# Kernel optimization log

Hardware: AMD Instinct MI355X
Metric: run time of the kernel (lower is better)

The kernel has to match this reference:

```python
import jax, jax.numpy as jnp
import numpy as np

N = 50000        # nodes
E = 800000       # random edges (plus N self-loops added in setup)
DIN = 128        # input_dim
H = 128          # hidden_dim
L = 3            # num_layers
EPS = 1e-5       # BatchNorm1d eps


def _bn(x, gamma, beta):
    # BatchNorm1d in training mode: batch stats over node axis, biased variance
    m = x.mean(axis=0)
    v = jnp.mean((x - m) ** 2, axis=0)
    return (x - m) * jax.lax.rsqrt(v + EPS) * gamma + beta


def setup_inputs() -> dict:
    key = jax.random.key(0)
    ks = jax.random.split(key, 11)
    feats = jax.random.normal(ks[0], (N, DIN), dtype=jnp.float32)
    # edge list with self-loops so every node has degree >= 1 (average pooling divides by degree)
    loops = jnp.arange(N, dtype=jnp.int64)
    src = jnp.concatenate([jax.random.randint(ks[1], (E,), 0, N, dtype=jnp.int64), loops])
    dst = jnp.concatenate([jax.random.randint(ks[2], (E,), 0, N, dtype=jnp.int64), loops])
    s = 0.05
    # per-layer MLP params (num_mlp_layers=2: Linear -> BN -> ReLU -> Linear), layer 0 has DIN==H
    W1 = jax.random.normal(ks[3], (L, DIN, H), dtype=jnp.float32) * s
    b1 = jnp.zeros((L, H), jnp.float32)
    g1 = jnp.ones((L, H), jnp.float32)
    be1 = jnp.zeros((L, H), jnp.float32)
    W2 = jax.random.normal(ks[4], (L, H, H), dtype=jnp.float32) * s
    b2 = jnp.zeros((L, H), jnp.float32)
    # outer BatchNorm1d per GNN layer
    og = jnp.ones((L, H), jnp.float32)
    ob = jnp.zeros((L, H), jnp.float32)
    return {"feats": feats, "W1": W1, "b1": b1, "g1": g1, "be1": be1,
            "W2": W2, "b2": b2, "og": og, "ob": ob, "src": src, "dst": dst}


def reference(feats, W1, b1, g1, be1, W2, b2, og, ob, src, dst):
    n = feats.shape[0]
    # degree = spmm(Adj, ones) -- constant across layers
    deg = jax.ops.segment_sum(jnp.ones(src.shape, jnp.float32), dst, num_segments=n)[:, None]
    h = feats
    for l in range(L):
        # pooled = spmm(Adj, h) via edge gather + segment reduce, then 'average' normalize
        pooled = jax.ops.segment_sum(h[src], dst, num_segments=n) / deg
        # GIN-style 2-layer MLP: Linear -> BN -> ReLU -> Linear
        z = jax.nn.relu(_bn(pooled @ W1[l] + b1[l], g1[l], be1[l]))
        z = z @ W2[l] + b2[l]
        # outer BatchNorm + ReLU
        h = jax.nn.relu(_bn(z, og[l], ob[l]))
    return h
```

## Files before the change

### kernel.cpp

```cpp
#include <hip/hip_runtime.h>
#include <hip/hip_bf16.h>
#include <stdint.h>

typedef _Float16 h16;
typedef h16 h16x2 __attribute__((ext_vector_type(2)));
typedef h16 h16x8 __attribute__((ext_vector_type(8)));
typedef float f32x4 __attribute__((ext_vector_type(4)));

#define HF 128
#define EPS 1e-5f
#define BSH 9
#define BROWS 512
#define BCAP 16384
#define ECHUNK 8192
#define SBANKS 8

union pk32 { uint32_t u; h16x2 h; };

static __device__ __forceinline__ uint32_t pack_h16(float a, float b) {
    pk32 c;
    c.h[0] = (h16)a; c.h[1] = (h16)b;
    return c.u;
}

static __device__ __forceinline__ float sum8(const float* __restrict__ st, int idx) {
    float s = 0.f;
#pragma unroll
    for (int b = 0; b < SBANKS; b++) s += st[b * 256 + idx];
    return s;
}


__global__ __launch_bounds__(256) void k_bscatter(const int* __restrict__ src,
                                                  const int* __restrict__ dst,
                                                  int* __restrict__ gcursor,
                                                  int2* __restrict__ staging, int ne, int nb) {
    __shared__ int h[128], gb[128];
    const int tid = threadIdx.x;
    if (tid < nb) h[tid] = 0;
    __syncthreads();
    const int beg = blockIdx.x * ECHUNK;
    const int end = min(beg + ECHUNK, ne);
    for (int i = beg + tid; i < end; i += 256)
        atomicAdd(&h[dst[i] >> BSH], 1);
    __syncthreads();
    if (tid < nb) {
        int c = h[tid];
        gb[tid] = c ? atomicAdd(&gcursor[tid], c) : 0;
        h[tid] = 0;
    }
    __syncthreads();
    for (int i = beg + tid; i < end; i += 256) {
        int d = dst[i];
        int b = d >> BSH;
        int r = atomicAdd(&h[b], 1);
        staging[(size_t)b * BCAP + gb[b] + r] = make_int2(src[i], d);
    }
}

__global__ __launch_bounds__(256) void k_bbuild(const int2* __restrict__ staging,
                                                const int* __restrict__ gcursor,
                                                int* __restrict__ rowbeg,
                                                int* __restrict__ rowend,
                                                float* __restrict__ deginv,
                                                int* __restrict__ csrsrc, int n) {
    __shared__ int hist[BROWS];
    __shared__ int scan[BROWS];
    const int b = blockIdx.x;
    const int tid = threadIdx.x;
    const int rb = b << BSH;
    const int nrows = min(BROWS, n - rb);
    const int base = b * BCAP;
    const int cnt = gcursor[b];
    hist[tid] = 0; hist[tid + 256] = 0;
    __syncthreads();
    for (int i = tid; i < cnt; i += 256)
        atomicAdd(&hist[staging[base + i].y - rb], 1);
    __syncthreads();
    const int i0 = tid, i1 = tid + 256;
    scan[i0] = hist[i0]; scan[i1] = hist[i1];
    __syncthreads();
    for (int off = 1; off < BROWS; off <<= 1) {
        int v0 = (i0 >= off) ? scan[i0 - off] : 0;
        int v1 = (i1 >= off) ? scan[i1 - off] : 0;
        __syncthreads();
        scan[i0] += v0; scan[i1] += v1;
        __syncthreads();
    }
    for (int r = tid; r < BROWS; r += 256) {
        int c = hist[r];
        int excl = scan[r] - c;
        if (r < nrows) {
            rowbeg[rb + r] = base + excl;
            rowend[rb + r] = base + excl + c;
            deginv[rb + r] = c ? 1.0f / (float)c : 0.f;
        }
        scan[r] = excl;
    }
    __syncthreads();
    for (int i = tid; i < cnt; i += 256) {
        int2 e = staging[base + i];
        int pos = atomicAdd(&scan[e.y - rb], 1);
        csrsrc[base + pos] = e.x;
    }
}

__global__ __launch_bounds__(256) void k_prep(const float* __restrict__ W1,
                                              const float* __restrict__ W2,
                                              h16* __restrict__ wp,
                                              const float* __restrict__ feats,
                                              uint32_t* __restrict__ hbuf, long tot2) {
    const int bid = (int)blockIdx.x;
    if (bid < 384) {
        const int mat = bid >> 6;
        const int idx = ((bid & 63) << 8) + (int)threadIdx.x;
        const int l = mat >> 1;
        const float* Wsrc = (mat & 1) ? (W2 + l * 16384) : (W1 + l * 16384);
        const int nn = idx >> 7, k = idx & 127;
        float w = Wsrc[k * 128 + nn];
        int pos = nn * 128 + ((((k >> 3) ^ (nn & 7))) << 3) + (k & 7);
        wp[mat * 16384 + pos] = (h16)w;
    } else {
        long i = (long)(bid - 384) * 256 + threadIdx.x;
        if (i < tot2) {
            float2 v = ((const float2*)feats)[i];
            hbuf[i] = pack_h16(v.x, v.y);
        }
    }
}

template <int AFF>
__global__ __launch_bounds__(256) void k_spmm(const uint32_t* __restrict__ hp,
                                              const int* __restrict__ rowbeg,
                                              const int* __restrict__ rowend,
                                              const float* __restrict__ deginv,
                                              const float* __restrict__ st,
                                              const float* __restrict__ g,
                                              const float* __restrict__ be,
                                              float inv_n,
                                              const int* __restrict__ csrsrc,
                                              uint32_t* __restrict__ pooled, int n, int np) {
    const int wid  = (int)((blockIdx.x * 256u + threadIdx.x) >> 6);
    const int lane = threadIdx.x & 63;
    if (wid >= np) return;
    const int gg = lane >> 4;
    const int fl = lane & 15;
    uint4* outrow = (uint4*)(pooled + (size_t)wid * 64);
    if (wid >= n) {
        if (gg == 0) outrow[fl] = make_uint4(0u, 0u, 0u, 0u);
        return;
    }

    uint32_t sv[4], cv[4];
    if (AFF) {
        const int c0 = lane * 2, c1 = c0 + 1;
        float m0 = sum8(st, c0) * inv_n, v0 = sum8(st, 128 + c0) * inv_n - m0 * m0;
        float sx = g[c0] * rsqrtf(v0 + EPS), cx = be[c0] - m0 * sx;
        float m1 = sum8(st, c1) * inv_n, v1 = sum8(st, 128 + c1) * inv_n - m1 * m1;
        float sy = g[c1] * rsqrtf(v1 + EPS), cy = be[c1] - m1 * sy;
        uint32_t su = pack_h16(sx, sy);
        uint32_t cu = pack_h16(cx, cy);
#pragma unroll
        for (int w = 0; w < 4; w++) {
            sv[w] = (uint32_t)__shfl((int)su, fl * 4 + w);
            cv[w] = (uint32_t)__shfl((int)cu, fl * 4 + w);
        }
    }

    const h16 z0 = (h16)0.f;
    h16x2 acc[4];
#pragma unroll
    for (int w = 0; w < 4; w++) acc[w] = (h16x2)z0;

    const int beg = rowbeg[wid], end = rowend[wid];
    for (int base = beg; base < end; base += 64) {
        const int rem = end - base;
        const int cnt = rem < 64 ? rem : 64;
        const int off = lane < cnt ? lane : cnt - 1;
        const int idx = csrsrc[base + off];
        for (int j = 0; j < cnt; j += 32) {
            uint4 p[8];
#pragma unroll
            for (int u = 0; u < 8; u++) {
                const int eb = j + u * 4;
                if (eb < cnt) {
                    int ge = eb + gg;
                    int gec = ge < cnt ? ge : cnt - 1;
                    int s = __shfl(idx, gec);
                    p[u] = *(const uint4*)(hp + (size_t)s * 64 + (fl << 2));
                }
            }
#pragma unroll
            for (int u = 0; u < 8; u++) {
                const int eb = j + u * 4;
                if (eb < cnt) {
                    const uint32_t* pw = (const uint32_t*)&p[u];
                    h16x2 v[4];
#pragma unroll
                    for (int w = 0; w < 4; w++) {
                        pk32 t; t.u = pw[w];
                        h16x2 x = t.h;
                        if (AFF) {
                            pk32 s2; s2.u = sv[w];
                            pk32 c2; c2.u = cv[w];
                            x = x * s2.h + c2.h;
                            x[0] = x[0] > z0 ? x[0] : z0;
                            x[1] = x[1] > z0 ? x[1] : z0;
                        }
                        v[w] = x;
                    }
                    if (eb + gg < cnt) {
#pragma unroll
                        for (int w = 0; w < 4; w++) acc[w] = acc[w] + v[w];
                    }
                }
            }
        }
    }

#pragma unroll
    for (int w = 0; w < 4; w++) {
        pk32 t; t.h = acc[w];
        pk32 r1; r1.u = (uint32_t)__shfl_xor((int)t.u, 16);
        t.h = t.h + r1.h;
        pk32 r2; r2.u = (uint32_t)__shfl_xor((int)t.u, 32);
        t.h = t.h + r2.h;
        acc[w] = t.h;
    }

    const float di = deginv[wid];
    uint4 o;
    o.x = pack_h16((float)acc[0][0] * di, (float)acc[0][1] * di);
    o.y = pack_h16((float)acc[1][0] * di, (float)acc[1][1] * di);
    o.z = pack_h16((float)acc[2][0] * di, (float)acc[2][1] * di);
    o.w = pack_h16((float)acc[3][0] * di, (float)acc[3][1] * di);
    if (gg == 0) outrow[fl] = o;
}

template <int MODE>
__global__ __launch_bounds__(256) void k_gemm(const uint32_t* __restrict__ Ap,
                                              const h16* __restrict__ Wp,
                                              const float* __restrict__ bias,
                                              const float* __restrict__ st,
                                              const float* __restrict__ g,
                                              const float* __restrict__ be,
                                              float inv_n,
                                              h16* __restrict__ Y,
                                              float* __restrict__ outstats, int n) {
    __shared__ __align__(16) h16 WT[128 * 128];
    __shared__ float sred[4][128];
    __shared__ float sred2[4][128];
    __shared__ float aff[256];
    const int tid = threadIdx.x;
    const int wave = tid >> 6, lane = tid & 63;

    {
        const char* gsrc = (const char*)Wp + wave * 1024 + lane * 16;
        char* ldst = (char*)&WT[0] + wave * 1024;
#pragma unroll
        for (int i = 0; i < 8; i++) {
            __builtin_amdgcn_global_load_lds(
                (const __attribute__((address_space(1))) uint32_t*)(gsrc + i * 4096),
                (__attribute__((address_space(3))) uint32_t*)(ldst + i * 4096),
                16, 0, 0);
        }
    }
    if (MODE == 1 && tid < 128) {
        float m = sum8(st, tid) * inv_n;
        float v = sum8(st, 128 + tid) * inv_n - m * m;
        float a = g[tid] * rsqrtf(v + EPS);
        aff[tid] = a;
        aff[128 + tid] = be[tid] - m * a;
    }

    const int lrow = lane & 15, quad = lane >> 4;
    const int bx = (int)blockIdx.x * 128;
    int mb[2];
    mb[0] = bx + wave * 16;
    mb[1] = bx + 64 + wave * 16;

    h16x8 ah[2][4];
    uint4 araw[2][4];
#pragma unroll
    for (int rt = 0; rt < 2; rt++) {
        const uint32_t* arow = Ap + (size_t)(mb[rt] + lrow) * 64 + quad * 4;
#pragma unroll
        for (int kt = 0; kt < 4; kt++)
            araw[rt][kt] = *(const uint4*)(arow + kt * 16);
    }

    __syncthreads();

#pragma unroll
    for (int rt = 0; rt < 2; rt++) {
#pragma unroll
        for (int kt = 0; kt < 4; kt++) {
            if (MODE == 0) {
                ah[rt][kt] = *(const h16x8*)&araw[rt][kt];
            } else {
                const uint32_t* pw = (const uint32_t*)&araw[rt][kt];
                h16x8 t;
#pragma unroll
                for (int j2 = 0; j2 < 4; j2++) {
                    pk32 w; w.u = pw[j2];
                    int k = kt * 32 + quad * 8 + j2 * 2;
                    float x0 = fmaxf(fmaf((float)w.h[0], aff[k],     aff[128 + k]),     0.f);
                    float x1 = fmaxf(fmaf((float)w.h[1], aff[k + 1], aff[129 + k]), 0.f);
                    t[2 * j2]     = (h16)x0;
                    t[2 * j2 + 1] = (h16)x1;
                }
                ah[rt][kt] = t;
            }
        }
    }

    f32x4 acc[2][8];
#pragma unroll
    for (int rt = 0; rt < 2; rt++)
#pragma unroll
        for (int nt = 0; nt < 8; nt++) acc[rt][nt] = (f32x4){0.f, 0.f, 0.f, 0.f};

    const int sw = lrow & 7;
#pragma unroll
    for (int nt = 0; nt < 8; nt++) {
        const h16* wbase = &WT[(nt * 16 + lrow) * 128];
#pragma unroll
        for (int kt = 0; kt < 4; kt++) {
            h16x8 bh = *(const h16x8*)(wbase + (((4 * kt + quad) ^ sw) << 3));
#pragma unroll
            for (int rt = 0; rt < 2; rt++)
                acc[rt][nt] = __builtin_amdgcn_mfma_f32_16x16x32_f16(ah[rt][kt], bh, acc[rt][nt], 0, 0, 0);
        }
    }

#pragma unroll
    for (int nt = 0; nt < 8; nt++) {
        int col = nt * 16 + lrow;
        float bv = bias[col];
        float csum = 0.f, csq = 0.f;
#pragma unroll
        for (int rt = 0; rt < 2; rt++) {
#pragma unroll
            for (int r = 0; r < 4; r++) {
                int row = mb[rt] + quad * 4 + r;
                float yv = acc[rt][nt][r] + bv;
                Y[(size_t)row * 128 + col] = (h16)yv;
                if (row < n) { csum += yv; csq += yv * yv; }
            }
        }
        csum += __shfl_xor(csum, 16, 64); csum += __shfl_xor(csum, 32, 64);
        csq  += __shfl_xor(csq,  16, 64); csq  += __shfl_xor(csq,  32, 64);
        if (quad == 0) { sred[wave][col] = csum; sred2[wave][col] = csq; }
    }
    __syncthreads();
    if (tid < 128) {
        float s = sred[0][tid] + sred[1][tid] + sred[2][tid] + sred[3][tid];
        float q = sred2[0][tid] + sred2[1][tid] + sred2[2][tid] + sred2[3][tid];
        const int bank = (int)(blockIdx.x & (SBANKS - 1));
        atomicAdd(&outstats[bank * 256 + tid], s);
        atomicAdd(&outstats[bank * 256 + 128 + tid], q);
    }
}

__global__ __launch_bounds__(256) void k_bnrelu(const uint32_t* __restrict__ Z,
                                                const float* __restrict__ st,
                                                const float* __restrict__ g,
                                                const float* __restrict__ be,
                                                float inv_n,
                                                float* __restrict__ out, long tot2) {
    long i = (long)blockIdx.x * 256 + threadIdx.x;
    if (i >= tot2) return;
    int c = (int)((i * 2) & 127);
    float m0 = sum8(st, c) * inv_n,     v0 = sum8(st, 128 + c) * inv_n - m0 * m0;
    float a0 = g[c] * rsqrtf(v0 + EPS),     c0 = be[c] - m0 * a0;
    float m1 = sum8(st, c + 1) * inv_n, v1 = sum8(st, 129 + c) * inv_n - m1 * m1;
    float a1 = g[c + 1] * rsqrtf(v1 + EPS), c1 = be[c + 1] - m1 * a1;
    pk32 w; w.u = Z[i];
    float2 o;
    o.x = fmaxf(fmaf((float)w.h[0], a0, c0), 0.f);
    o.y = fmaxf(fmaf((float)w.h[1], a1, c1), 0.f);
    ((float2*)out)[i] = o;
}

extern "C" void kernel_launch(void* const* d_in, const int* in_sizes, int n_in,
                              void* d_out, int out_size, void* d_ws, size_t ws_size,
                              hipStream_t stream) {
    const float* feats = (const float*)d_in[0];
    const float* W1    = (const float*)d_in[1];
    const float* b1    = (const float*)d_in[2];
    const float* g1    = (const float*)d_in[3];
    const float* be1   = (const float*)d_in[4];
    const float* W2    = (const float*)d_in[5];
    const float* b2    = (const float*)d_in[6];
    const float* og    = (const float*)d_in[7];
    const float* ob    = (const float*)d_in[8];
    const int*   src   = (const int*)d_in[9];
    const int*   dst   = (const int*)d_in[10];

    const int n  = in_sizes[0] / HF;
    const int ne = in_sizes[9];
    const int np = (n + 127) & ~127;
    const int nb = (n + BROWS - 1) >> BSH;

    char* p = (char*)d_ws;
    auto alloc = [&](size_t bytes) -> char* {
        char* r = p;
        p += (bytes + 511) & ~(size_t)511;
        return r;
    };
    uint32_t* hbuf    = (uint32_t*)alloc((size_t)np * 64 * 4);
    uint32_t* pooled  = (uint32_t*)alloc((size_t)np * 64 * 4);
    uint32_t* ybuf    = (uint32_t*)alloc((size_t)np * 64 * 4);
    uint32_t* zb      = (uint32_t*)alloc((size_t)np * 64 * 4);
    h16*      wprep   = (h16*)     alloc(6 * 16384 * 2);
    float*    deginv  = (float*)   alloc((size_t)n * 4);
    int*      rowbeg  = (int*)     alloc((size_t)n * 4);
    int*      rowend  = (int*)     alloc((size_t)n * 4);
    int*      csrsrc  = (int*)     alloc((size_t)nb * BCAP * 4);
    int2*     staging = (int2*)    alloc((size_t)nb * BCAP * 8);
    char*     zone    = alloc(512 + 6 * SBANKS * 256 * 4);
    int*      gcursor = (int*)zone;
    float*    stats6  = (float*)(zone + 512);

    hipMemsetAsync(zone, 0, 512 + 6 * SBANKS * 256 * 4, stream);

    const long tot2  = (long)n * (HF / 2);
    const int bnb    = (int)((tot2 + 255) / 256);
    const int spmmb  = np / 4;
    const int gemmb  = np / 128;
    const float inv_n = 1.0f / (float)n;
    const int ebk = (ne + ECHUNK - 1) / ECHUNK;
    const int SL = SBANKS * 256;

    k_prep    <<<384 + bnb, 256, 0, stream>>>(W1, W2, wprep, feats, hbuf, tot2);
    k_bscatter<<<ebk, 256, 0, stream>>>(src, dst, gcursor, staging, ne, nb);
    k_bbuild  <<<nb, 256, 0, stream>>>(staging, gcursor, rowbeg, rowend, deginv, csrsrc, n);

    for (int l = 0; l < 3; l++) {
        float* sY = stats6 + (2 * l) * SL;
        float* sZ = stats6 + (2 * l + 1) * SL;
        if (l == 0)
            k_spmm<0><<<spmmb, 256, 0, stream>>>(hbuf, rowbeg, rowend, deginv,
                                                 nullptr, nullptr, nullptr, inv_n,
                                                 csrsrc, pooled, n, np);
        else
            k_spmm<1><<<spmmb, 256, 0, stream>>>(zb, rowbeg, rowend, deginv,
                                                 stats6 + (2 * (l - 1) + 1) * SL,
                                                 og + (l - 1) * HF, ob + (l - 1) * HF, inv_n,
                                                 csrsrc, pooled, n, np);
        k_gemm<0><<<gemmb, 256, 0, stream>>>(pooled,
                                             wprep + (size_t)(2 * l) * 16384,
                                             b1 + l * HF,
                                             nullptr, nullptr, nullptr, inv_n,
                                             (h16*)ybuf, sY, n);
        k_gemm<1><<<gemmb, 256, 0, stream>>>(ybuf,
                                             wprep + (size_t)(2 * l + 1) * 16384,
                                             b2 + l * HF,
                                             sY, g1 + l * HF, be1 + l * HF, inv_n,
                                             (h16*)zb, sZ, n);
    }
    k_bnrelu<<<bnb, 256, 0, stream>>>(zb, stats6 + 5 * SL, og + 2 * HF, ob + 2 * HF,
                                      inv_n, (float*)d_out, tot2);
}
```

Before: 375.0 us.

## Merge prep and edge-scatter kernels, split GEMM columns across 8 waves, vectorize BN

Folds the weight/feature conversion kernel and the edge bucket-scatter kernel into one launch, so one kernel launch goes away and the two independent jobs can run side by side. The GEMM kernels now run 512 threads per block. Each pair of waves shares a row group and splits the 128 output columns in half, which halves the accumulator registers per wave and adds parallelism per block. The cost is that both waves in a pair load the same A rows. The final BN+ReLU kernel now handles four features per thread with wider loads and stores.

```diff
diff --git a/kernel.cpp b/kernel.cpp
--- a/kernel.cpp
+++ b/kernel.cpp
@@ -30,31 +30,55 @@
     return s;
 }
 
-
-__global__ __launch_bounds__(256) void k_bscatter(const int* __restrict__ src,
+__global__ __launch_bounds__(256) void k_prepscat(const float* __restrict__ W1,
+                                                  const float* __restrict__ W2,
+                                                  h16* __restrict__ wp,
+                                                  const float* __restrict__ feats,
+                                                  uint32_t* __restrict__ hbuf, long tot2,
+                                                  const int* __restrict__ src,
                                                   const int* __restrict__ dst,
                                                   int* __restrict__ gcursor,
-                                                  int2* __restrict__ staging, int ne, int nb) {
+                                                  int2* __restrict__ staging, int ne, int nb,
+                                                  int ebk) {
     __shared__ int h[128], gb[128];
+    const int bid = (int)blockIdx.x;
     const int tid = threadIdx.x;
-    if (tid < nb) h[tid] = 0;
-    __syncthreads();
-    const int beg = blockIdx.x * ECHUNK;
-    const int end = min(beg + ECHUNK, ne);
-    for (int i = beg + tid; i < end; i += 256)
-        atomicAdd(&h[dst[i] >> BSH], 1);
-    __syncthreads();
-    if (tid < nb) {
-        int c = h[tid];
-        gb[tid] = c ? atomicAdd(&gcursor[tid], c) : 0;
-        h[tid] = 0;
-    }
-    __syncthreads();
-    for (int i = beg + tid; i < end; i += 256) {
-        int d = dst[i];
-        int b = d >> BSH;
-        int r = atomicAdd(&h[b], 1);
-        staging[(size_t)b * BCAP + gb[b] + r] = make_int2(src[i], d);
+    if (bid < ebk) {
+        if (tid < nb) h[tid] = 0;
+        __syncthreads();
+        const int beg = bid * ECHUNK;
+        const int end = min(beg + ECHUNK, ne);
+        for (int i = beg + tid; i < end; i += 256)
+            atomicAdd(&h[dst[i] >> BSH], 1);
+        __syncthreads();
+        if (tid < nb) {
+            int c = h[tid];
+            gb[tid] = c ? atomicAdd(&gcursor[tid], c) : 0;
+            h[tid] = 0;
+        }
+        __syncthreads();
+        for (int i = beg + tid; i < end; i += 256) {
+            int d = dst[i];
+            int b = d >> BSH;
+            int r = atomicAdd(&h[b], 1);
+            staging[(size_t)b * BCAP + gb[b] + r] = make_int2(src[i], d);
+        }
+    } else if (bid < ebk + 384) {
+        const int wb = bid - ebk;
+        const int mat = wb >> 6;
+        const int idx = ((wb & 63) << 8) + tid;
+        const int l = mat >> 1;
+        const float* Wsrc = (mat & 1) ? (W2 + l * 16384) : (W1 + l * 16384);
+        const int nn = idx >> 7, k = idx & 127;
+        float w = Wsrc[k * 128 + nn];
+        int pos = nn * 128 + ((((k >> 3) ^ (nn & 7))) << 3) + (k & 7);
+        wp[mat * 16384 + pos] = (h16)w;
+    } else {
+        long i = (long)(bid - ebk - 384) * 256 + tid;
+        if (i < tot2) {
+            float2 v = ((const float2*)feats)[i];
+            hbuf[i] = pack_h16(v.x, v.y);
+        }
     }
 }
 
@@ -102,30 +126,6 @@
         int2 e = staging[base + i];
         int pos = atomicAdd(&scan[e.y - rb], 1);
         csrsrc[base + pos] = e.x;
-    }
-}
-
-__global__ __launch_bounds__(256) void k_prep(const float* __restrict__ W1,
-                                              const float* __restrict__ W2,
-                                              h16* __restrict__ wp,
-                                              const float* __restrict__ feats,
-                                              uint32_t* __restrict__ hbuf, long tot2) {
-    const int bid = (int)blockIdx.x;
-    if (bid < 384) {
-        const int mat = bid >> 6;
-        const int idx = ((bid & 63) << 8) + (int)threadIdx.x;
-        const int l = mat >> 1;
-        const float* Wsrc = (mat & 1) ? (W2 + l * 16384) : (W1 + l * 16384);
-        const int nn = idx >> 7, k = idx & 127;
-        float w = Wsrc[k * 128 + nn];
-        int pos = nn * 128 + ((((k >> 3) ^ (nn & 7))) << 3) + (k & 7);
-        wp[mat * 16384 + pos] = (h16)w;
-    } else {
-        long i = (long)(bid - 384) * 256 + threadIdx.x;
-        if (i < tot2) {
-            float2 v = ((const float2*)feats)[i];
-            hbuf[i] = pack_h16(v.x, v.y);
-        }
     }
 }
 
@@ -238,7 +238,7 @@
 }
 
 template <int MODE>
-__global__ __launch_bounds__(256) void k_gemm(const uint32_t* __restrict__ Ap,
+__global__ __launch_bounds__(512) void k_gemm(const uint32_t* __restrict__ Ap,
                                               const h16* __restrict__ Wp,
                                               const float* __restrict__ bias,
                                               const float* __restrict__ st,
@@ -258,10 +258,10 @@
         const char* gsrc = (const char*)Wp + wave * 1024 + lane * 16;
         char* ldst = (char*)&WT[0] + wave * 1024;
 #pragma unroll
-        for (int i = 0; i < 8; i++) {
+        for (int i = 0; i < 4; i++) {
             __builtin_amdgcn_global_load_lds(
-                (const __attribute__((address_space(1))) uint32_t*)(gsrc + i * 4096),
-                (__attribute__((address_space(3))) uint32_t*)(ldst + i * 4096),
+                (const __attribute__((address_space(1))) uint32_t*)(gsrc + i * 8192),
+                (__attribute__((address_space(3))) uint32_t*)(ldst + i * 8192),
                 16, 0, 0);
         }
     }
@@ -274,10 +274,11 @@
     }
 
     const int lrow = lane & 15, quad = lane >> 4;
+    const int rg = wave >> 1, nh = wave & 1;
     const int bx = (int)blockIdx.x * 128;
     int mb[2];
-    mb[0] = bx + wave * 16;
-    mb[1] = bx + 64 + wave * 16;
+    mb[0] = bx + rg * 16;
+    mb[1] = bx + 64 + rg * 16;
 
     h16x8 ah[2][4];
     uint4 araw[2][4];
@@ -314,16 +315,17 @@
         }
     }
 
-    f32x4 acc[2][8];
+    f32x4 acc[2][4];
 #pragma unroll
     for (int rt = 0; rt < 2; rt++)
 #pragma unroll
-        for (int nt = 0; nt < 8; nt++) acc[rt][nt] = (f32x4){0.f, 0.f, 0.f, 0.f};
+        for (int nt = 0; nt < 4; nt++) acc[rt][nt] = (f32x4){0.f, 0.f, 0.f, 0.f};
 
     const int sw = lrow & 7;
 #pragma unroll
-    for (int nt = 0; nt < 8; nt++) {
-        const h16* wbase = &WT[(nt * 16 + lrow) * 128];
+    for (int nt = 0; nt < 4; nt++) {
+        const int ntg = nh * 4 + nt;
+        const h16* wbase = &WT[(ntg * 16 + lrow) * 128];
 #pragma unroll
         for (int kt = 0; kt < 4; kt++) {
             h16x8 bh = *(const h16x8*)(wbase + (((4 * kt + quad) ^ sw) << 3));
@@ -334,8 +336,8 @@
     }
 
 #pragma unroll
-    for (int nt = 0; nt < 8; nt++) {
-        int col = nt * 16 + lrow;
+    for (int nt = 0; nt < 4; nt++) {
+        int col = (nh * 4 + nt) * 16 + lrow;
         float bv = bias[col];
         float csum = 0.f, csq = 0.f;
 #pragma unroll
@@ -350,7 +352,7 @@
         }
         csum += __shfl_xor(csum, 16, 64); csum += __shfl_xor(csum, 32, 64);
         csq  += __shfl_xor(csq,  16, 64); csq  += __shfl_xor(csq,  32, 64);
-        if (quad == 0) { sred[wave][col] = csum; sred2[wave][col] = csq; }
+        if (quad == 0) { sred[rg][col] = csum; sred2[rg][col] = csq; }
     }
     __syncthreads();
     if (tid < 128) {
@@ -367,19 +369,27 @@
                                                 const float* __restrict__ g,
                                                 const float* __restrict__ be,
                                                 float inv_n,
-                                                float* __restrict__ out, long tot2) {
+                                                float* __restrict__ out, long tot4) {
     long i = (long)blockIdx.x * 256 + threadIdx.x;
-    if (i >= tot2) return;
-    int c = (int)((i * 2) & 127);
-    float m0 = sum8(st, c) * inv_n,     v0 = sum8(st, 128 + c) * inv_n - m0 * m0;
-    float a0 = g[c] * rsqrtf(v0 + EPS),     c0 = be[c] - m0 * a0;
-    float m1 = sum8(st, c + 1) * inv_n, v1 = sum8(st, 129 + c) * inv_n - m1 * m1;
-    float a1 = g[c + 1] * rsqrtf(v1 + EPS), c1 = be[c + 1] - m1 * a1;
-    pk32 w; w.u = Z[i];
-    float2 o;
-    o.x = fmaxf(fmaf((float)w.h[0], a0, c0), 0.f);
-    o.y = fmaxf(fmaf((float)w.h[1], a1, c1), 0.f);
-    ((float2*)out)[i] = o;
+    if (i >= tot4) return;
+    int c = (int)((i * 4) & 127);
+    float a[4], cc[4];
+#pragma unroll
+    for (int j = 0; j < 4; j++) {
+        float m = sum8(st, c + j) * inv_n;
+        float v = sum8(st, 128 + c + j) * inv_n - m * m;
+        a[j] = g[c + j] * rsqrtf(v + EPS);
+        cc[j] = be[c + j] - m * a[j];
+    }
+    uint2 w2 = ((const uint2*)Z)[i];
+    pk32 w0; w0.u = w2.x;
+    pk32 w1; w1.u = w2.y;
+    float4 o;
+    o.x = fmaxf(fmaf((float)w0.h[0], a[0], cc[0]), 0.f);
+    o.y = fmaxf(fmaf((float)w0.h[1], a[1], cc[1]), 0.f);
+    o.z = fmaxf(fmaf((float)w1.h[0], a[2], cc[2]), 0.f);
+    o.w = fmaxf(fmaf((float)w1.h[1], a[3], cc[3]), 0.f);
+    ((float4*)out)[i] = o;
 }
 
 extern "C" void kernel_launch(void* const* d_in, const int* in_sizes, int n_in,
@@ -425,15 +435,17 @@
     hipMemsetAsync(zone, 0, 512 + 6 * SBANKS * 256 * 4, stream);
 
     const long tot2  = (long)n * (HF / 2);
+    const long tot4  = tot2 / 2;
     const int bnb    = (int)((tot2 + 255) / 256);
+    const int bnb4   = (int)((tot4 + 255) / 256);
     const int spmmb  = np / 4;
     const int gemmb  = np / 128;
     const float inv_n = 1.0f / (float)n;
     const int ebk = (ne + ECHUNK - 1) / ECHUNK;
     const int SL = SBANKS * 256;
 
-    k_prep    <<<384 + bnb, 256, 0, stream>>>(W1, W2, wprep, feats, hbuf, tot2);
-    k_bscatter<<<ebk, 256, 0, stream>>>(src, dst, gcursor, staging, ne, nb);
+    k_prepscat<<<ebk + 384 + bnb, 256, 0, stream>>>(W1, W2, wprep, feats, hbuf, tot2,
+                                                    src, dst, gcursor, staging, ne, nb, ebk);
     k_bbuild  <<<nb, 256, 0, stream>>>(staging, gcursor, rowbeg, rowend, deginv, csrsrc, n);
 
     for (int l = 0; l < 3; l++) {
@@ -448,17 +460,17 @@
                                                  stats6 + (2 * (l - 1) + 1) * SL,
                                                  og + (l - 1) * HF, ob + (l - 1) * HF, inv_n,
                                                  csrsrc, pooled, n, np);
-        k_gemm<0><<<gemmb, 256, 0, stream>>>(pooled,
+        k_gemm<0><<<gemmb, 512, 0, stream>>>(pooled,
                                              wprep + (size_t)(2 * l) * 16384,
                                              b1 + l * HF,
                                              nullptr, nullptr, nullptr, inv_n,
                                              (h16*)ybuf, sY, n);
-        k_gemm<1><<<gemmb, 256, 0, stream>>>(ybuf,
+        k_gemm<1><<<gemmb, 512, 0, stream>>>(ybuf,
                                              wprep + (size_t)(2 * l + 1) * 16384,
                                              b2 + l * HF,
                                              sY, g1 + l * HF, be1 + l * HF, inv_n,
                                              (h16*)zb, sZ, n);
     }
-    k_bnrelu<<<bnb, 256, 0, stream>>>(zb, stats6 + 5 * SL, og + 2 * HF, ob + 2 * HF,
-                                      inv_n, (float*)d_out, tot2);
-}
+    k_bnrelu<<<bnb4, 256, 0, stream>>>(zb, stats6 + 5 * SL, og + 2 * HF, ob + 2 * HF,
+                                       inv_n, (float*)d_out, tot4);
+}
```

New measurement: 346.2 us. 7.7% less time.
